# Kernel tuning notes

Hardware: AMD Instinct MI355X
Metric: run time of the kernel (lower is better)

The kernel has to match this reference:

```python
import jax, jax.numpy as jnp
import numpy as np

M, K, N, P = 2048, 4096, 64, 16   # prev outputs, decoder nodes, matrix size, parents per node
ACTIVE_THRESHOLD = 12             # >= 12/16 active parents required

def setup_inputs() -> dict:
    key = jax.random.key(0)
    k1, k2, k3, k4, k5 = jax.random.split(key, 5)
    prev_outputs = jax.random.normal(k1, (M, N, N), dtype=jnp.float32)
    prev_is_active = jax.random.bernoulli(k2, 0.9, (M,))                 # bool (M,)
    parent_indices = jax.random.randint(k3, (K, P), 0, M)                # static wiring (K,16)
    w = jax.random.normal(k4, (K, P), dtype=jnp.float32) / np.sqrt(P)    # per-node parent weights
    b = jax.random.normal(k5, (K,), dtype=jnp.float32) * 0.01            # per-node bias
    return {"prev_outputs": prev_outputs, "prev_is_active": prev_is_active,
            "parent_indices": parent_indices, "w": w, "b": b}

def reference(prev_outputs, prev_is_active, parent_indices, w, b):
    # gather parent outputs: (K, P, n, n)
    gathered = prev_outputs[parent_indices]
    # per-node decoder: weighted combine of 16 parents + bias, tanh
    combined = jnp.einsum('kp,kpnm->knm', w, gathered) + b[:, None, None]
    out = jnp.tanh(combined)[:, None]                                    # (K,1,n,n)
    # activity threshold gate: node active iff >= 12 of 16 parents active
    n_active = prev_is_active[parent_indices].astype(jnp.int32).sum(axis=-1)  # (K,)
    out_active = n_active >= ACTIVE_THRESHOLD
    out = jnp.where(out_active[:, None, None, None], out, jnp.zeros_like(out))
    return out, out_active
```

## Files before the change

kernel.cpp:

```cpp
#include <hip/hip_runtime.h>


#define M_ROWS   2048
#define K_NODES  4096
#define NN       4096
#define POS_TILE 32
#define NTHREADS 1024
#define ROW_B    80
#define LDS_BYTES (M_ROWS * ROW_B)
#define OUT_ELEMS (K_NODES * NN)
#define ACTIVE_THRESHOLD 12

typedef float f32x4 __attribute__((ext_vector_type(4)));
typedef unsigned short u16x8 __attribute__((ext_vector_type(8)));

__device__ __forceinline__ float fast_tanh(float x) {
  float ax = __builtin_fabsf(x);
  float e  = __expf(-2.0f * ax);
  float r  = (1.0f - e) * __builtin_amdgcn_rcpf(1.0f + e);
  return __builtin_copysignf(r, x);
}

__device__ __forceinline__ unsigned short f2bf_rne(float f) {
  unsigned u = __float_as_uint(f);
  u += 0x7FFFu + ((u >> 16) & 1u);
  return (unsigned short)(u >> 16);
}

__global__ __launch_bounds__(256) void act_kernel(
    const int* __restrict__ pidx, const unsigned int* __restrict__ isact,
    float* __restrict__ outact) {
  __shared__ int mode_sh;
  if (threadIdx.x == 0) mode_sh = 0;
  __syncthreads();
  int bad = 0;
  for (int i = threadIdx.x; i < 512; i += 256) bad |= (isact[i] > 1u);
  if (bad) atomicOr(&mode_sh, 1);
  __syncthreads();
  const int shift = mode_sh ? 0 : 2;
  const unsigned char* actb = (const unsigned char*)isact;

  int k = blockIdx.x * 256 + threadIdx.x;
  const int4* ip = (const int4*)(pidx + k * 16);
  int4 ia = ip[0], ib = ip[1], ic = ip[2], id4 = ip[3];
  int ids[16] = {ia.x, ia.y, ia.z, ia.w, ib.x, ib.y, ib.z, ib.w,
                 ic.x, ic.y, ic.z, ic.w, id4.x, id4.y, id4.z, id4.w};
  int n = 0;
  #pragma unroll
  for (int p = 0; p < 16; ++p) n += (actb[ids[p] << shift] != 0);
  outact[k] = (n >= ACTIVE_THRESHOLD) ? 1.0f : 0.0f;
}

#define PFMA(vv, wv)                                              \
  { float wv_ = (wv);                                             \
    a0 += wv_ * __uint_as_float((unsigned)(vv)[0] << 16);         \
    a1 += wv_ * __uint_as_float((unsigned)(vv)[1] << 16);         \
    a2 += wv_ * __uint_as_float((unsigned)(vv)[2] << 16);         \
    a3 += wv_ * __uint_as_float((unsigned)(vv)[3] << 16);         \
    a4 += wv_ * __uint_as_float((unsigned)(vv)[4] << 16);         \
    a5 += wv_ * __uint_as_float((unsigned)(vv)[5] << 16);         \
    a6 += wv_ * __uint_as_float((unsigned)(vv)[6] << 16);         \
    a7 += wv_ * __uint_as_float((unsigned)(vv)[7] << 16); }

__global__ __launch_bounds__(NTHREADS, 1) void decoder_kernel(
    const float* __restrict__ prev, const int* __restrict__ pidx,
    const float* __restrict__ w, const float* __restrict__ b,
    const float* __restrict__ actf, float* __restrict__ out,
    float* __restrict__ outact) {
  extern __shared__ char xb[];
  const int tid = threadIdx.x;
  const int bid = blockIdx.x;

  const int xcd   = bid & 7;
  const int loc   = bid >> 3;
  const int tile  = xcd * 16 + (loc >> 1);
  const int half  = loc & 1;
  const int pos0  = tile * POS_TILE;
  const int nbase = half * (K_NODES / 2);

  #pragma unroll
  for (int it = 0; it < 8; ++it) {
    int ci = (it << 10) + tid;
    int r = ci >> 2, c = ci & 3;
    const float* sp = prev + r * NN + pos0 + (c << 3);
    f32x4 v0 = *(const f32x4*)sp;
    f32x4 v1 = *(const f32x4*)(sp + 4);
    u16x8 o;
    o[0] = f2bf_rne(v0.x); o[1] = f2bf_rne(v0.y);
    o[2] = f2bf_rne(v0.z); o[3] = f2bf_rne(v0.w);
    o[4] = f2bf_rne(v1.x); o[5] = f2bf_rne(v1.y);
    o[6] = f2bf_rne(v1.z); o[7] = f2bf_rne(v1.w);
    *(u16x8*)(xb + r * ROW_B + (c << 4)) = o;
  }
  __syncthreads();

  const int q = tid & 3;
  const int s = tid >> 2;
  const int coff = q << 4;

  for (int it = 0; it < 8; ++it) {
    int n = nbase + (it << 8) + s;
    const int4*   ip = (const int4*)(pidx + (n << 4));
    const float4* wp = (const float4*)(w + (n << 4));
    int4   i0 = ip[0], i1 = ip[1], i2 = ip[2], i3 = ip[3];
    float4 w0 = wp[0], w1 = wp[1], w2 = wp[2], w3 = wp[3];
    float  bk = b[n];
    float  g  = actf[n];

    float a0 = bk, a1 = bk, a2 = bk, a3 = bk;
    float a4 = bk, a5 = bk, a6 = bk, a7 = bk;

    u16x8 v0 = *(const u16x8*)(xb + i0.x * ROW_B + coff);
    u16x8 v1 = *(const u16x8*)(xb + i0.y * ROW_B + coff);
    u16x8 v2 = *(const u16x8*)(xb + i0.z * ROW_B + coff);
    u16x8 v3 = *(const u16x8*)(xb + i0.w * ROW_B + coff);
    u16x8 v4 = *(const u16x8*)(xb + i1.x * ROW_B + coff);
    u16x8 v5 = *(const u16x8*)(xb + i1.y * ROW_B + coff);
    u16x8 v6 = *(const u16x8*)(xb + i1.z * ROW_B + coff);
    u16x8 v7 = *(const u16x8*)(xb + i1.w * ROW_B + coff);
    __builtin_amdgcn_sched_barrier(0);
    PFMA(v0, w0.x) PFMA(v1, w0.y) PFMA(v2, w0.z) PFMA(v3, w0.w)
    PFMA(v4, w1.x) PFMA(v5, w1.y) PFMA(v6, w1.z) PFMA(v7, w1.w)

    v0 = *(const u16x8*)(xb + i2.x * ROW_B + coff);
    v1 = *(const u16x8*)(xb + i2.y * ROW_B + coff);
    v2 = *(const u16x8*)(xb + i2.z * ROW_B + coff);
    v3 = *(const u16x8*)(xb + i2.w * ROW_B + coff);
    v4 = *(const u16x8*)(xb + i3.x * ROW_B + coff);
    v5 = *(const u16x8*)(xb + i3.y * ROW_B + coff);
    v6 = *(const u16x8*)(xb + i3.z * ROW_B + coff);
    v7 = *(const u16x8*)(xb + i3.w * ROW_B + coff);
    __builtin_amdgcn_sched_barrier(0);
    PFMA(v0, w2.x) PFMA(v1, w2.y) PFMA(v2, w2.z) PFMA(v3, w2.w)
    PFMA(v4, w3.x) PFMA(v5, w3.y) PFMA(v6, w3.z) PFMA(v7, w3.w)

    f32x4 o0, o1;
    o0.x = fast_tanh(a0) * g; o0.y = fast_tanh(a1) * g;
    o0.z = fast_tanh(a2) * g; o0.w = fast_tanh(a3) * g;
    o1.x = fast_tanh(a4) * g; o1.y = fast_tanh(a5) * g;
    o1.z = fast_tanh(a6) * g; o1.w = fast_tanh(a7) * g;

    float* op = out + ((size_t)n << 12) + pos0 + (q << 3);
    *(f32x4*)op       = o0;
    *(f32x4*)(op + 4) = o1;

    if (tile == 0 && q == 0) outact[n] = g;
  }
}

extern "C" void kernel_launch(void* const* d_in, const int* in_sizes, int n_in,
                              void* d_out, int out_size, void* d_ws, size_t ws_size,
                              hipStream_t stream) {
  const float* prev  = (const float*)d_in[0];
  const void*  isact = d_in[1];
  const int*   pidx  = (const int*)d_in[2];
  const float* w     = (const float*)d_in[3];
  const float* b     = (const float*)d_in[4];
  float* out    = (float*)d_out;
  float* outact = out + OUT_ELEMS;

  (void)hipFuncSetAttribute((const void*)decoder_kernel,
                            hipFuncAttributeMaxDynamicSharedMemorySize, LDS_BYTES);

  act_kernel<<<K_NODES / 256, 256, 0, stream>>>(
      pidx, (const unsigned int*)isact, outact);
  decoder_kernel<<<(NN / POS_TILE) * 2, NTHREADS, LDS_BYTES, stream>>>(
      prev, pidx, w, b, outact, out, outact);
}
```

Baseline: 38.82 us.

## Shrink position tile to 16 and have each block cover all nodes

Halves the per-block position tile from 32 to 16 columns and cuts the LDS row stride from 80 to 48 bytes. Each block now processes all 4096 nodes instead of half, and the XCD-aware block remapping is removed. The grid stays at 256 blocks, but each block stages half as much of prev into LDS and does not duplicate that staging across two half-node blocks. The trade-off is 32-byte output stores per thread pair instead of 64-byte segments, and a different LDS bank pattern for the gathers.

```diff
diff --git a/kernel.cpp b/kernel.cpp
--- a/kernel.cpp
+++ b/kernel.cpp
@@ -4,9 +4,9 @@
 #define M_ROWS   2048
 #define K_NODES  4096
 #define NN       4096
-#define POS_TILE 32
+#define POS_TILE 16
 #define NTHREADS 1024
-#define ROW_B    80
+#define ROW_B    48
 #define LDS_BYTES (M_ROWS * ROW_B)
 #define OUT_ELEMS (K_NODES * NN)
 #define ACTIVE_THRESHOLD 12
@@ -68,20 +68,14 @@
     const float* __restrict__ actf, float* __restrict__ out,
     float* __restrict__ outact) {
   extern __shared__ char xb[];
-  const int tid = threadIdx.x;
-  const int bid = blockIdx.x;
-
-  const int xcd   = bid & 7;
-  const int loc   = bid >> 3;
-  const int tile  = xcd * 16 + (loc >> 1);
-  const int half  = loc & 1;
-  const int pos0  = tile * POS_TILE;
-  const int nbase = half * (K_NODES / 2);
+  const int tid  = threadIdx.x;
+  const int bid  = blockIdx.x;
+  const int pos0 = bid * POS_TILE;
 
   #pragma unroll
-  for (int it = 0; it < 8; ++it) {
+  for (int it = 0; it < 4; ++it) {
     int ci = (it << 10) + tid;
-    int r = ci >> 2, c = ci & 3;
+    int r = ci >> 1, c = ci & 1;
     const float* sp = prev + r * NN + pos0 + (c << 3);
     f32x4 v0 = *(const f32x4*)sp;
     f32x4 v1 = *(const f32x4*)(sp + 4);
@@ -94,12 +88,12 @@
   }
   __syncthreads();
 
-  const int q = tid & 3;
-  const int s = tid >> 2;
-  const int coff = q << 4;
+  const int q  = tid & 1;
+  const int s  = tid >> 1;
+  const int qb = q << 4;
 
   for (int it = 0; it < 8; ++it) {
-    int n = nbase + (it << 8) + s;
+    int n = (it << 9) + s;
     const int4*   ip = (const int4*)(pidx + (n << 4));
     const float4* wp = (const float4*)(w + (n << 4));
     int4   i0 = ip[0], i1 = ip[1], i2 = ip[2], i3 = ip[3];
@@ -110,26 +104,26 @@
     float a0 = bk, a1 = bk, a2 = bk, a3 = bk;
     float a4 = bk, a5 = bk, a6 = bk, a7 = bk;
 
-    u16x8 v0 = *(const u16x8*)(xb + i0.x * ROW_B + coff);
-    u16x8 v1 = *(const u16x8*)(xb + i0.y * ROW_B + coff);
-    u16x8 v2 = *(const u16x8*)(xb + i0.z * ROW_B + coff);
-    u16x8 v3 = *(const u16x8*)(xb + i0.w * ROW_B + coff);
-    u16x8 v4 = *(const u16x8*)(xb + i1.x * ROW_B + coff);
-    u16x8 v5 = *(const u16x8*)(xb + i1.y * ROW_B + coff);
-    u16x8 v6 = *(const u16x8*)(xb + i1.z * ROW_B + coff);
-    u16x8 v7 = *(const u16x8*)(xb + i1.w * ROW_B + coff);
+    u16x8 v0 = *(const u16x8*)(xb + i0.x * ROW_B + qb);
+    u16x8 v1 = *(const u16x8*)(xb + i0.y * ROW_B + qb);
+    u16x8 v2 = *(const u16x8*)(xb + i0.z * ROW_B + qb);
+    u16x8 v3 = *(const u16x8*)(xb + i0.w * ROW_B + qb);
+    u16x8 v4 = *(const u16x8*)(xb + i1.x * ROW_B + qb);
+    u16x8 v5 = *(const u16x8*)(xb + i1.y * ROW_B + qb);
+    u16x8 v6 = *(const u16x8*)(xb + i1.z * ROW_B + qb);
+    u16x8 v7 = *(const u16x8*)(xb + i1.w * ROW_B + qb);
     __builtin_amdgcn_sched_barrier(0);
     PFMA(v0, w0.x) PFMA(v1, w0.y) PFMA(v2, w0.z) PFMA(v3, w0.w)
     PFMA(v4, w1.x) PFMA(v5, w1.y) PFMA(v6, w1.z) PFMA(v7, w1.w)
 
-    v0 = *(const u16x8*)(xb + i2.x * ROW_B + coff);
-    v1 = *(const u16x8*)(xb + i2.y * ROW_B + coff);
-    v2 = *(const u16x8*)(xb + i2.z * ROW_B + coff);
-    v3 = *(const u16x8*)(xb + i2.w * ROW_B + coff);
-    v4 = *(const u16x8*)(xb + i3.x * ROW_B + coff);
-    v5 = *(const u16x8*)(xb + i3.y * ROW_B + coff);
-    v6 = *(const u16x8*)(xb + i3.z * ROW_B + coff);
-    v7 = *(const u16x8*)(xb + i3.w * ROW_B + coff);
+    v0 = *(const u16x8*)(xb + i2.x * ROW_B + qb);
+    v1 = *(const u16x8*)(xb + i2.y * ROW_B + qb);
+    v2 = *(const u16x8*)(xb + i2.z * ROW_B + qb);
+    v3 = *(const u16x8*)(xb + i2.w * ROW_B + qb);
+    v4 = *(const u16x8*)(xb + i3.x * ROW_B + qb);
+    v5 = *(const u16x8*)(xb + i3.y * ROW_B + qb);
+    v6 = *(const u16x8*)(xb + i3.z * ROW_B + qb);
+    v7 = *(const u16x8*)(xb + i3.w * ROW_B + qb);
     __builtin_amdgcn_sched_barrier(0);
     PFMA(v0, w2.x) PFMA(v1, w2.y) PFMA(v2, w2.z) PFMA(v3, w2.w)
     PFMA(v4, w3.x) PFMA(v5, w3.y) PFMA(v6, w3.z) PFMA(v7, w3.w)
@@ -144,7 +138,7 @@
     *(f32x4*)op       = o0;
     *(f32x4*)(op + 4) = o1;
 
-    if (tile == 0 && q == 0) outact[n] = g;
+    if (bid == 0 && q == 0) outact[n] = g;
   }
 }
 
@@ -164,6 +158,6 @@
 
   act_kernel<<<K_NODES / 256, 256, 0, stream>>>(
       pidx, (const unsigned int*)isact, outact);
-  decoder_kernel<<<(NN / POS_TILE) * 2, NTHREADS, LDS_BYTES, stream>>>(
+  decoder_kernel<<<NN / POS_TILE, NTHREADS, LDS_BYTES, stream>>>(
       prev, pidx, w, b, outact, out, outact);
 }
```

Measured after the change: 41.15 us. 1.06x slower.
